# Optimization experiments

Hardware: AMD Instinct MI355X
Metric: run time of the kernel (lower is better)

## Reference

```python
import math
import jax, jax.numpy as jnp
import numpy as np

EPS = 1.0
TAU = 0.95
KAPPA = (1.0 - TAU) / 2.0
XI = (1.0 - TAU) / (1.0 + TAU)
RHO = EPS * TAU / (1.0 - TAU)
NUM_ITER = 10
B, H, WD, CC = 4, 128, 512, 64


def setup_inputs() -> dict:
    key = jax.random.key(0)
    C = jax.random.normal(key, (B, H, WD, CC), dtype=jnp.float32)
    return {"C": C}


def _lse(x, axis):
    return jax.nn.logsumexp(x, axis=axis)


def _softmax_lse(Cm, f, g, axis):
    # S = (C - f[...,None] - g[...,None,:]) / eps ; return eps*logsumexp(-S, axis)
    S = (Cm - f[..., None] - g[..., None, :]) / EPS
    return EPS * _lse(-S, axis)


def _lse_kernel(Cm, f, g, axis):
    w_res = _softmax_lse(Cm, f, g, axis)
    w_sgn = f if axis == -1 else g
    return w_res - jnp.where(jnp.isfinite(w_sgn), w_sgn, jnp.zeros_like(w_sgn))


def _sinkhorn_update(Cm, f, g, axis, log_marginal):
    app = _lse_kernel(Cm, f, g, axis)
    return EPS * log_marginal - jnp.where(jnp.isfinite(app), app, jnp.zeros_like(app))


def _smin(h, log_marginal):
    # smin(h, c) = -rho * logsumexp(-h/rho + log c, axis=-1)
    return -RHO * _lse(-h / RHO + log_marginal, -1)


def reference(C):
    b, h, wd, cc = C.shape
    log_a = jnp.full((wd,), -math.log(wd), dtype=C.dtype)  # row marginal (uniform)
    log_b = jnp.full((cc,), -math.log(cc), dtype=C.dtype)  # col marginal (uniform)

    # init potentials
    f = -EPS * _lse(-C / EPS + log_b, -1)       # (B,H,W)
    g = jnp.zeros((b, h, cc), dtype=C.dtype)    # (B,H,C)

    for _ in range(NUM_ITER):
        old_f = f
        new_g = TAU * _sinkhorn_update(C, old_f, g, -2, log_b)
        new_g = new_g - KAPPA * _smin(old_f, log_a)[..., None]
        new_g = new_g + XI * _smin(new_g, log_b)[..., None]
        new_f = TAU * _sinkhorn_update(C, f, new_g, -1, log_a)
        new_f = new_f - KAPPA * _smin(new_g, log_b)[..., None]
        new_f = new_f + XI * _smin(new_f, log_a)[..., None]
        f, g = new_f, new_g

    S = (C - f[..., None] - g[..., None, :]) / EPS
    return jnp.exp(-S)
```

## Files before the change

kernel.cpp:

```cpp
#include <hip/hip_runtime.h>
#include <hip/hip_fp16.h>


#define WD_ 512
#define CC_ 64
#define NITER_ 10
#define LPH 72

__global__ __launch_bounds__(512, 4)
void uot_sinkhorn_kernel(const float* __restrict__ C, float* __restrict__ out) {
    constexpr float TAU   = 0.95f;
    constexpr float KAPPA = 0.025f;
    constexpr float XI    = 0.05f / 1.95f;
    constexpr float RHO   = 19.0f;
    constexpr float INV_RHO = 1.0f / 19.0f;
    const float log_a = -6.2383246250395075f;
    const float log_b = -4.1588830833596715f;

    __shared__ __align__(16) unsigned short Es[WD_ * LPH];
    __shared__ __align__(16) float vsb[8 * CC_];
    __shared__ __align__(16) float ps[2][WD_];
    __shared__ __align__(16) float red[2][8];

    const int tid  = threadIdx.x;
    const int lane = tid & 63;
    const int wv   = tid >> 6;
    const int r    = lane >> 4;
    const int cg   = lane & 15;
    const int w0   = wv * 64;

    const size_t base = (size_t)blockIdx.x * (WD_ * CC_);
    const float4* Cg4   = reinterpret_cast<const float4*>(C + base);
    float4*       outg4 = reinterpret_cast<float4*>(out + base);

    #pragma unroll
    for (int i = 0; i < 16; ++i) {
        int fi = i * 512 + tid;
        float4 v = Cg4[fi];
        int w  = fi >> 4;
        int c0 = (fi & 15) << 2;
        __half2 h0 = __floats2half2_rn(__expf(-v.x), __expf(-v.y));
        __half2 h1 = __floats2half2_rn(__expf(-v.z), __expf(-v.w));
        uint2 pk;
        *reinterpret_cast<__half2*>(&pk.x) = h0;
        *reinterpret_cast<__half2*>(&pk.y) = h1;
        *reinterpret_cast<uint2*>(&Es[w * LPH + c0]) = pk;
    }
    __syncthreads();

    float4 ER[16];
    #pragma unroll
    for (int k = 0; k < 16; ++k) {
        uint2 raw = *reinterpret_cast<const uint2*>(&Es[tid * LPH + 4 * k]);
        float2 a = __half22float2(*reinterpret_cast<__half2*>(&raw.x));
        float2 b = __half22float2(*reinterpret_cast<__half2*>(&raw.y));
        ER[k] = make_float4(a.x, a.y, b.x, b.y);
    }

    float u_own;
    {
        float s0 = 0.f, s1 = 0.f, s2 = 0.f, s3 = 0.f;
        #pragma unroll
        for (int k = 0; k < 16; ++k) {
            s0 += ER[k].x; s1 += ER[k].y; s2 += ER[k].z; s3 += ER[k].w;
        }
        float fv = -(log_b + __logf((s0 + s1) + (s2 + s3)));
        u_own = __expf(fv);
        float x = __expf(-fv * INV_RHO);
        #pragma unroll
        for (int off = 32; off > 0; off >>= 1) x += __shfl_xor(x, off, 64);
        if (lane == 0) red[0][wv] = x;
    }

    float xi_eff = 0.0f;

    #pragma unroll 2
    for (int it = 0; it < NITER_; ++it) {
        const int p = it & 1;

        float ax = 0.f, ay = 0.f, az = 0.f, aw = 0.f;
        #pragma unroll
        for (int j = 0; j < 16; ++j) {
            int row = w0 + 4 * j + r;
            float uw = __shfl(u_own, 4 * j + r, 64);
            uint2 raw = *reinterpret_cast<const uint2*>(&Es[row * LPH + 4 * cg]);
            float2 a = __half22float2(*reinterpret_cast<__half2*>(&raw.x));
            float2 b = __half22float2(*reinterpret_cast<__half2*>(&raw.y));
            ax = fmaf(uw, a.x, ax); ay = fmaf(uw, a.y, ay);
            az = fmaf(uw, b.x, az); aw = fmaf(uw, b.y, aw);
        }
        ax += __shfl_xor(ax, 16, 64); ay += __shfl_xor(ay, 16, 64);
        az += __shfl_xor(az, 16, 64); aw += __shfl_xor(aw, 16, 64);
        ax += __shfl_xor(ax, 32, 64); ay += __shfl_xor(ay, 32, 64);
        az += __shfl_xor(az, 32, 64); aw += __shfl_xor(aw, 32, 64);
        if (lane < 16)
            *reinterpret_cast<float4*>(&ps[p][w0 + 4 * cg]) =
                make_float4(ax, ay, az, aw);

        __syncthreads();

        float R = ((red[p][0] + red[p][1]) + (red[p][2] + red[p][3]))
                + ((red[p][4] + red[p][5]) + (red[p][6] + red[p][7]));
        float sminF2 = -RHO * (log_a + __logf(R));
        float shift  = xi_eff * sminF2;
        float sminF  = shift + sminF2;
        float S = 0.f;
        #pragma unroll
        for (int k = 0; k < 8; ++k) S += ps[p][k * 64 + lane];
        float appg = __logf(S) + shift;
        float ng2  = TAU * (log_b - appg) - KAPPA * sminF;
        float t = __expf(-ng2 * INV_RHO);
        #pragma unroll
        for (int off = 32; off > 0; off >>= 1) t += __shfl_xor(t, off, 64);
        float sminG2 = -RHO * (log_b + __logf(t));
        vsb[w0 + lane] = __expf(ng2 + XI * sminG2);
        float sminG = (1.0f + XI) * sminG2;

        float s0 = 0.f, s1 = 0.f, s2 = 0.f, s3 = 0.f;
        #pragma unroll
        for (int k = 0; k < 16; ++k) {
            float4 v4 = *reinterpret_cast<const float4*>(&vsb[w0 + 4 * k]);
            s0 = fmaf(v4.x, ER[k].x, s0); s1 = fmaf(v4.y, ER[k].y, s1);
            s2 = fmaf(v4.z, ER[k].z, s2); s3 = fmaf(v4.w, ER[k].w, s3);
        }
        float appf = __logf((s0 + s1) + (s2 + s3));
        float nf2  = TAU * (log_a - appf) - KAPPA * sminG;
        u_own = __expf(nf2);
        float x = __expf(-nf2 * INV_RHO);
        #pragma unroll
        for (int off = 32; off > 0; off >>= 1) x += __shfl_xor(x, off, 64);
        if (lane == 0) red[p ^ 1][wv] = x;
        xi_eff = XI;
    }

    __syncthreads();
    {
        float R = ((red[0][0] + red[0][1]) + (red[0][2] + red[0][3]))
                + ((red[0][4] + red[0][5]) + (red[0][6] + red[0][7]));
        float sminF2 = -RHO * (log_a + __logf(R));
        ps[1][tid] = u_own * __expf(XI * sminF2);
    }
    __syncthreads();

    #pragma unroll
    for (int i = 0; i < 16; ++i) {
        int fi = i * 512 + tid;
        int w  = fi >> 4;
        int c0 = (fi & 15) << 2;
        float uw = ps[1][w];
        float4 vv = *reinterpret_cast<const float4*>(&vsb[w0 + c0]);
        uint2 raw = *reinterpret_cast<const uint2*>(&Es[w * LPH + c0]);
        float2 a = __half22float2(*reinterpret_cast<__half2*>(&raw.x));
        float2 b = __half22float2(*reinterpret_cast<__half2*>(&raw.y));
        float4 o;
        o.x = uw * vv.x * a.x; o.y = uw * vv.y * a.y;
        o.z = uw * vv.z * b.x; o.w = uw * vv.w * b.y;
        outg4[fi] = o;
    }
}

extern "C" void kernel_launch(void* const* d_in, const int* in_sizes, int n_in,
                              void* d_out, int out_size, void* d_ws, size_t ws_size,
                              hipStream_t stream) {
    const float* C = (const float*)d_in[0];
    float* out = (float*)d_out;
    uot_sinkhorn_kernel<<<dim3(512), dim3(512), 0, stream>>>(C, out);
}
```

Measured before the change: 154.4 us.

## Transpose exp(-C) tile in LDS and use packed fp16 dot2 for reductions

Stores exp(-C) in LDS transposed (channel-major, padded stride) so each lane can reduce a column over contiguous rows, replacing the shuffle-based column reduction. Keeps the register-resident row copy as packed half2 and uses the fp16 dot2 builtin for both the row and column matvecs. The scaling vectors u and v are stored in fp16 in shared memory. The XI shift on v is folded algebraically into the f update and a final combined scale, and the per-wave partial-sum arrays are replaced by a full xs buffer. In exchange it adds fp16 rounding of the potentials, scattered 2-byte LDS writes during the transposed fill, and an extra barrier per iteration.

Result: faster. 127.8 us (-17.2%).

```diff
diff --git a/kernel.cpp b/kernel.cpp
--- a/kernel.cpp
+++ b/kernel.cpp
@@ -1,11 +1,17 @@
 #include <hip/hip_runtime.h>
-#include <hip/hip_fp16.h>
 
+
+typedef _Float16 h2 __attribute__((ext_vector_type(2)));
+typedef _Float16 h4 __attribute__((ext_vector_type(4)));
 
 #define WD_ 512
 #define CC_ 64
 #define NITER_ 10
-#define LPH 72
+#define ETS 516
+
+__device__ __forceinline__ float fdot2(h2 a, h2 b, float c) {
+    return __builtin_amdgcn_fdot2(a, b, c, false);
+}
 
 __global__ __launch_bounds__(512, 4)
 void uot_sinkhorn_kernel(const float* __restrict__ C, float* __restrict__ out) {
@@ -13,20 +19,19 @@
     constexpr float KAPPA = 0.025f;
     constexpr float XI    = 0.05f / 1.95f;
     constexpr float RHO   = 19.0f;
-    constexpr float INV_RHO = 1.0f / 19.0f;
+    constexpr float IR    = 1.0f / 19.0f;
     const float log_a = -6.2383246250395075f;
     const float log_b = -4.1588830833596715f;
 
-    __shared__ __align__(16) unsigned short Es[WD_ * LPH];
-    __shared__ __align__(16) float vsb[8 * CC_];
-    __shared__ __align__(16) float ps[2][WD_];
-    __shared__ __align__(16) float red[2][8];
+    __shared__ __align__(16) _Float16 ET[CC_ * ETS];
+    __shared__ __align__(16) _Float16 us_h[WD_];
+    __shared__ __align__(16) _Float16 vsb[WD_];
+    __shared__ __align__(16) float    ps[WD_];
+    __shared__ __align__(16) float    xs[WD_];
 
     const int tid  = threadIdx.x;
     const int lane = tid & 63;
     const int wv   = tid >> 6;
-    const int r    = lane >> 4;
-    const int cg   = lane & 15;
     const int w0   = wv * 64;
 
     const size_t base = (size_t)blockIdx.x * (WD_ * CC_);
@@ -39,122 +44,118 @@
         float4 v = Cg4[fi];
         int w  = fi >> 4;
         int c0 = (fi & 15) << 2;
-        __half2 h0 = __floats2half2_rn(__expf(-v.x), __expf(-v.y));
-        __half2 h1 = __floats2half2_rn(__expf(-v.z), __expf(-v.w));
-        uint2 pk;
-        *reinterpret_cast<__half2*>(&pk.x) = h0;
-        *reinterpret_cast<__half2*>(&pk.y) = h1;
-        *reinterpret_cast<uint2*>(&Es[w * LPH + c0]) = pk;
+        ET[(c0 + 0) * ETS + w] = (_Float16)__expf(-v.x);
+        ET[(c0 + 1) * ETS + w] = (_Float16)__expf(-v.y);
+        ET[(c0 + 2) * ETS + w] = (_Float16)__expf(-v.z);
+        ET[(c0 + 3) * ETS + w] = (_Float16)__expf(-v.w);
     }
     __syncthreads();
 
-    float4 ER[16];
+    h2 ER[32];
     #pragma unroll
-    for (int k = 0; k < 16; ++k) {
-        uint2 raw = *reinterpret_cast<const uint2*>(&Es[tid * LPH + 4 * k]);
-        float2 a = __half22float2(*reinterpret_cast<__half2*>(&raw.x));
-        float2 b = __half22float2(*reinterpret_cast<__half2*>(&raw.y));
-        ER[k] = make_float4(a.x, a.y, b.x, b.y);
+    for (int k = 0; k < 32; ++k) {
+        h2 e; e[0] = ET[(2 * k) * ETS + tid]; e[1] = ET[(2 * k + 1) * ETS + tid];
+        ER[k] = e;
     }
 
-    float u_own;
     {
+        const h2 ones = { (_Float16)1.0f, (_Float16)1.0f };
         float s0 = 0.f, s1 = 0.f, s2 = 0.f, s3 = 0.f;
         #pragma unroll
-        for (int k = 0; k < 16; ++k) {
-            s0 += ER[k].x; s1 += ER[k].y; s2 += ER[k].z; s3 += ER[k].w;
+        for (int k = 0; k < 32; k += 4) {
+            s0 = fdot2(ER[k + 0], ones, s0); s1 = fdot2(ER[k + 1], ones, s1);
+            s2 = fdot2(ER[k + 2], ones, s2); s3 = fdot2(ER[k + 3], ones, s3);
         }
         float fv = -(log_b + __logf((s0 + s1) + (s2 + s3)));
-        u_own = __expf(fv);
-        float x = __expf(-fv * INV_RHO);
-        #pragma unroll
-        for (int off = 32; off > 0; off >>= 1) x += __shfl_xor(x, off, 64);
-        if (lane == 0) red[0][wv] = x;
+        us_h[tid] = (_Float16)__expf(fv);
+        xs[tid]   = __expf(-fv * IR);
     }
+    __syncthreads();
 
     float xi_eff = 0.0f;
+    float sminG2_last = 0.0f;
 
-    #pragma unroll 2
     for (int it = 0; it < NITER_; ++it) {
-        const int p = it & 1;
+        float a0 = 0.f, a1 = 0.f, a2 = 0.f, a3 = 0.f;
+        #pragma unroll
+        for (int j = 0; j < 16; j += 2) {
+            h4 e0 = *reinterpret_cast<const h4*>(&ET[lane * ETS + w0 + 4 * j]);
+            h4 u0 = *reinterpret_cast<const h4*>(&us_h[w0 + 4 * j]);
+            h4 e1 = *reinterpret_cast<const h4*>(&ET[lane * ETS + w0 + 4 * j + 4]);
+            h4 u1 = *reinterpret_cast<const h4*>(&us_h[w0 + 4 * j + 4]);
+            h2 ea = {e0[0], e0[1]}, eb = {e0[2], e0[3]};
+            h2 ua = {u0[0], u0[1]}, ub = {u0[2], u0[3]};
+            h2 ec = {e1[0], e1[1]}, ed = {e1[2], e1[3]};
+            h2 uc = {u1[0], u1[1]}, ud = {u1[2], u1[3]};
+            a0 = fdot2(ea, ua, a0); a1 = fdot2(eb, ub, a1);
+            a2 = fdot2(ec, uc, a2); a3 = fdot2(ed, ud, a3);
+        }
+        ps[tid] = (a0 + a1) + (a2 + a3);
 
-        float ax = 0.f, ay = 0.f, az = 0.f, aw = 0.f;
+        float r = 0.f;
         #pragma unroll
-        for (int j = 0; j < 16; ++j) {
-            int row = w0 + 4 * j + r;
-            float uw = __shfl(u_own, 4 * j + r, 64);
-            uint2 raw = *reinterpret_cast<const uint2*>(&Es[row * LPH + 4 * cg]);
-            float2 a = __half22float2(*reinterpret_cast<__half2*>(&raw.x));
-            float2 b = __half22float2(*reinterpret_cast<__half2*>(&raw.y));
-            ax = fmaf(uw, a.x, ax); ay = fmaf(uw, a.y, ay);
-            az = fmaf(uw, b.x, az); aw = fmaf(uw, b.y, aw);
-        }
-        ax += __shfl_xor(ax, 16, 64); ay += __shfl_xor(ay, 16, 64);
-        az += __shfl_xor(az, 16, 64); aw += __shfl_xor(aw, 16, 64);
-        ax += __shfl_xor(ax, 32, 64); ay += __shfl_xor(ay, 32, 64);
-        az += __shfl_xor(az, 32, 64); aw += __shfl_xor(aw, 32, 64);
-        if (lane < 16)
-            *reinterpret_cast<float4*>(&ps[p][w0 + 4 * cg]) =
-                make_float4(ax, ay, az, aw);
+        for (int k = 0; k < 8; ++k) r += xs[k * 64 + lane];
+        #pragma unroll
+        for (int off = 32; off > 0; off >>= 1) r += __shfl_xor(r, off, 64);
 
         __syncthreads();
 
-        float R = ((red[p][0] + red[p][1]) + (red[p][2] + red[p][3]))
-                + ((red[p][4] + red[p][5]) + (red[p][6] + red[p][7]));
-        float sminF2 = -RHO * (log_a + __logf(R));
+        float sminF2 = -RHO * (log_a + __logf(r));
         float shift  = xi_eff * sminF2;
         float sminF  = shift + sminF2;
         float S = 0.f;
         #pragma unroll
-        for (int k = 0; k < 8; ++k) S += ps[p][k * 64 + lane];
+        for (int k = 0; k < 8; ++k) S += ps[k * 64 + lane];
         float appg = __logf(S) + shift;
         float ng2  = TAU * (log_b - appg) - KAPPA * sminF;
-        float t = __expf(-ng2 * INV_RHO);
+        vsb[tid] = (_Float16)__expf(ng2);
+        float t = __expf(-ng2 * IR);
         #pragma unroll
         for (int off = 32; off > 0; off >>= 1) t += __shfl_xor(t, off, 64);
         float sminG2 = -RHO * (log_b + __logf(t));
-        vsb[w0 + lane] = __expf(ng2 + XI * sminG2);
-        float sminG = (1.0f + XI) * sminG2;
 
         float s0 = 0.f, s1 = 0.f, s2 = 0.f, s3 = 0.f;
         #pragma unroll
-        for (int k = 0; k < 16; ++k) {
-            float4 v4 = *reinterpret_cast<const float4*>(&vsb[w0 + 4 * k]);
-            s0 = fmaf(v4.x, ER[k].x, s0); s1 = fmaf(v4.y, ER[k].y, s1);
-            s2 = fmaf(v4.z, ER[k].z, s2); s3 = fmaf(v4.w, ER[k].w, s3);
+        for (int q = 0; q < 16; q += 2) {
+            h4 vb0 = *reinterpret_cast<const h4*>(&vsb[w0 + 4 * q]);
+            h4 vb1 = *reinterpret_cast<const h4*>(&vsb[w0 + 4 * q + 4]);
+            h2 va = {vb0[0], vb0[1]}, vbb = {vb0[2], vb0[3]};
+            h2 vc = {vb1[0], vb1[1]}, vd  = {vb1[2], vb1[3]};
+            s0 = fdot2(ER[2 * q + 0], va,  s0);
+            s1 = fdot2(ER[2 * q + 1], vbb, s1);
+            s2 = fdot2(ER[2 * q + 2], vc,  s2);
+            s3 = fdot2(ER[2 * q + 3], vd,  s3);
         }
         float appf = __logf((s0 + s1) + (s2 + s3));
-        float nf2  = TAU * (log_a - appf) - KAPPA * sminG;
-        u_own = __expf(nf2);
-        float x = __expf(-nf2 * INV_RHO);
-        #pragma unroll
-        for (int off = 32; off > 0; off >>= 1) x += __shfl_xor(x, off, 64);
-        if (lane == 0) red[p ^ 1][wv] = x;
+        float nf2  = TAU * (log_a - appf - XI * sminG2)
+                   - KAPPA * (1.0f + XI) * sminG2;
+        float u_own = __expf(nf2);
+        us_h[tid] = (_Float16)u_own;
+        xs[tid]   = __expf(-nf2 * IR);
         xi_eff = XI;
+        sminG2_last = sminG2;
+        __syncthreads();
     }
 
-    __syncthreads();
-    {
-        float R = ((red[0][0] + red[0][1]) + (red[0][2] + red[0][3]))
-                + ((red[0][4] + red[0][5]) + (red[0][6] + red[0][7]));
-        float sminF2 = -RHO * (log_a + __logf(R));
-        ps[1][tid] = u_own * __expf(XI * sminF2);
-    }
-    __syncthreads();
+    float r = 0.f;
+    #pragma unroll
+    for (int k = 0; k < 8; ++k) r += xs[k * 64 + lane];
+    #pragma unroll
+    for (int off = 32; off > 0; off >>= 1) r += __shfl_xor(r, off, 64);
+    float sminF2 = -RHO * (log_a + __logf(r));
+    const float SUV = __expf(XI * (sminF2 + sminG2_last));
 
     #pragma unroll
     for (int i = 0; i < 16; ++i) {
         int fi = i * 512 + tid;
         int w  = fi >> 4;
         int c0 = (fi & 15) << 2;
-        float uw = ps[1][w];
-        float4 vv = *reinterpret_cast<const float4*>(&vsb[w0 + c0]);
-        uint2 raw = *reinterpret_cast<const uint2*>(&Es[w * LPH + c0]);
-        float2 a = __half22float2(*reinterpret_cast<__half2*>(&raw.x));
-        float2 b = __half22float2(*reinterpret_cast<__half2*>(&raw.y));
+        float uf = SUV * (float)us_h[w];
         float4 o;
-        o.x = uw * vv.x * a.x; o.y = uw * vv.y * a.y;
-        o.z = uw * vv.z * b.x; o.w = uw * vv.w * b.y;
+        o.x = uf * (float)vsb[w0 + c0 + 0] * (float)ET[(c0 + 0) * ETS + w];
+        o.y = uf * (float)vsb[w0 + c0 + 1] * (float)ET[(c0 + 1) * ETS + w];
+        o.z = uf * (float)vsb[w0 + c0 + 2] * (float)ET[(c0 + 2) * ETS + w];
+        o.w = uf * (float)vsb[w0 + c0 + 3] * (float)ET[(c0 + 3) * ETS + w];
         outg4[fi] = o;
     }
 }
```
